# Kernel tuning notes

Hardware: AMD Instinct MI355X
Metric: run time of the kernel (lower is better)

The kernel has to match this reference:

```python
import jax, jax.numpy as jnp
import numpy as np

RADIUS = 5
KS = 2 * RADIUS - 1          # kernel_size = 9
PAD = KS // 2                # 4
CENTER = RADIUS - 1          # 4 (== PAD)
EPS = 1e-10


def _offsets_and_kernel():
    # Distance kernel exactly as torch.meshgrid(indexing='ij') in the module;
    # the center entry is skipped in the loop, so drop it here.
    yy, xx = np.meshgrid(np.arange(KS), np.arange(KS), indexing='ij')
    dist = np.sqrt((xx - CENTER) ** 2 + (yy - CENTER) ** 2).astype(np.float32)
    keep = ~((yy == CENTER) & (xx == CENTER))
    return (yy[keep].astype(np.int32), xx[keep].astype(np.int32), dist[keep])


def setup_inputs() -> dict:
    key = jax.random.key(0)
    target = (jax.random.uniform(key, (5, 2048, 2048)) < 0.15).astype(jnp.float32)
    return {"target": target}


def reference(target):
    # target: [5, H, W] binary float masks
    H, W = target.shape[1], target.shape[2]
    feature_weight = jnp.sum(target, axis=0)                      # [H, W]
    combined = (feature_weight > 0).astype(jnp.float32)           # [H, W]

    padded = jnp.pad(combined, PAD, mode='edge')                  # replicate pad
    oi, oj, kv = _offsets_and_kernel()
    offs = (jnp.asarray(oi), jnp.asarray(oj), jnp.asarray(kv))

    def body(min_d, off):
        i, j, k = off
        shifted = jax.lax.dynamic_slice(padded, (i, j), (H, W))
        diff = (shifted != combined).astype(jnp.float32)
        d = jnp.where(diff > 0, k / (diff + EPS), jnp.inf)
        return jnp.minimum(min_d, d), None

    min_d, _ = jax.lax.scan(body, jnp.full((H, W), jnp.inf, jnp.float32), offs)

    contour = jnp.where(jnp.isfinite(min_d), 1.0 / (min_d + EPS), 0.0)
    w = (feature_weight + contour) ** 2
    w = (w - w.min()) / (w.max() - w.min() + EPS)
    return w * combined
```

## Files before the change

### kernel.cpp

```cpp
#include <hip/hip_runtime.h>
#include <math.h>
#include <utility>

static constexpr int HH = 2048;
static constexpr int WW = 2048;
static constexpr int NPIX = HH * WW;
static constexpr int HPR = WW / 16;
static constexpr int TW = 256;
static constexpr int TH = 64;
static constexpr int GX = WW / TW;
static constexpr int GY = HH / TH;

template <typename F, int... Is>
__device__ __forceinline__ void sf_impl(F&& f, std::integer_sequence<int, Is...>) {
    (f(std::integral_constant<int, Is>{}), ...);
}
template <int N, typename F>
__device__ __forceinline__ void static_for(F&& f) {
    sf_impl(f, std::make_integer_sequence<int, N>{});
}

__host__ __device__ constexpr int rank_of(int d2) {
    switch (d2) {
        case 1:  return 1;  case 2:  return 2;  case 4:  return 3;
        case 5:  return 4;  case 8:  return 5;  case 9:  return 6;
        case 10: return 7;  case 13: return 8;  case 16: return 9;
        case 17: return 10; case 18: return 11; case 20: return 12;
        case 25: return 13; case 32: return 14;
    }
    return 0;
}

__device__ const int D2S[16] = {0, 1, 2, 4, 5, 8, 9, 10, 13, 16, 17, 18, 20, 25, 32, 0};

__device__ __forceinline__ unsigned long long spread8(unsigned int b) {
    unsigned long long t = (unsigned long long)b * 0x0101010101010101ull;
    t &= 0x8040201008040201ull;
    return ((t + 0x7f7f7f7f7f7f7f7full) >> 7) & 0x0101010101010101ull;
}

__global__ __launch_bounds__(512) void k_packdist(const float* __restrict__ t,
                                                  ulonglong2* __restrict__ code16,
                                                  unsigned long long* __restrict__ obs_blk) {
    __shared__ unsigned pkt[TH + 8][9];
    __shared__ unsigned char fwt[TH][TW];
    __shared__ unsigned long long swl[8], swh[8];

    const int bx = blockIdx.x & (GX - 1);
    const int by = blockIdx.x >> 3;
    const int tx0 = bx * TW, ty0 = by * TH;
    const int wid = threadIdx.x >> 6, lane = threadIdx.x & 63;

#pragma unroll 5
    for (int it = wid * 45; it < wid * 45 + 45; ++it) {
        const int r = it / 5;
        const int s = it - 5 * r;
        const bool active = (s < 4) | (lane < 8);
        const int c = (s < 4) ? (64 * s - 4 + lane) : (252 + lane);
        const int gy = min(max(ty0 + r - 4, 0), HH - 1);
        const int gx = min(max(tx0 + c, 0), WW - 1);
        float s5 = 0.f;
        if (active) {
            const int o = gy * WW + gx;
            s5 = t[o] + t[NPIX + o] + t[2 * NPIX + o] + t[3 * NPIX + o]
               + t[4 * NPIX + o];
        }
        const unsigned long long bal = __ballot(active && (s5 > 0.f));
        if (lane == 0) {
            if (s < 4) {
                pkt[r][2 * s]     = (unsigned)bal;
                pkt[r][2 * s + 1] = (unsigned)(bal >> 32);
            } else {
                pkt[r][8] = (unsigned)bal;
            }
        }
        const int rr = r - 4;
        if (active && rr >= 0 && rr < TH && c >= 0 && c < TW)
            fwt[rr][c] = (unsigned char)(int)s5;
    }
    __syncthreads();

    unsigned long long obl = 0, obh = 0;
#pragma unroll
    for (int k = 0; k < 2; ++k) {
        const int ch = threadIdx.x + k * 512;
        const int rr = ch >> 4;
        const int cx = ch & 15;
        const int x0 = cx * 16;
        const int w0 = x0 >> 5;
        const int sh = x0 & 31;

        unsigned acc[15];
        static_for<15>([&](auto I) { acc[I.value] = 0u; });

        const unsigned long long Wc =
            ((unsigned long long)pkt[rr + 4][w0]
           | ((unsigned long long)pkt[rr + 4][w0 + 1] << 32)) >> sh;
        const unsigned C = (unsigned)(Wc >> 4);

        static_for<9>([&](auto DY) {
            constexpr int dyi = DY.value;
            constexpr int dy = dyi - 4;
            const unsigned long long W = (dyi == 4) ? Wc :
                (((unsigned long long)pkt[rr + dyi][w0]
                | ((unsigned long long)pkt[rr + dyi][w0 + 1] << 32)) >> sh);
            static_for<9>([&](auto DX) {
                constexpr int dx = DX.value - 4;
                if constexpr (!(dx == 0 && dy == 0)) {
                    constexpr int rk = rank_of(dy * dy + dx * dx);
                    const unsigned S = (unsigned)(W >> (4 + dx));
                    acc[rk] |= S ^ C;
                }
            });
        });

        unsigned found = 0, p0 = 0, p1 = 0, p2 = 0, p3 = 0;
        static_for<14>([&](auto RI) {
            constexpr int r = RI.value + 1;
            const unsigned nw = acc[r] & ~found;
            found |= acc[r];
            if constexpr (r & 1) p0 |= nw;
            if constexpr (r & 2) p1 |= nw;
            if constexpr (r & 4) p2 |= nw;
            if constexpr (r & 8) p3 |= nw;
        });

        const uint4 fvw = *(const uint4*)&fwt[rr][x0];
        const unsigned long long fv0 =
            (unsigned long long)fvw.x | ((unsigned long long)fvw.y << 32);
        const unsigned long long fv1 =
            (unsigned long long)fvw.z | ((unsigned long long)fvw.w << 32);

        unsigned long long cq0 = 0, cq1 = 0;
        static_for<2>([&](auto J) {
            constexpr int j = J.value;
            const unsigned long long f = j ? fv1 : fv0;
            const unsigned c0 = (p0 >> (8 * j)) & 0xff;
            const unsigned c1 = (p1 >> (8 * j)) & 0xff;
            const unsigned c2 = (p2 >> (8 * j)) & 0xff;
            const unsigned c3 = (p3 >> (8 * j)) & 0xff;
            const unsigned long long cls = spread8(c0) | (spread8(c1) << 1)
                                         | (spread8(c2) << 2) | (spread8(c3) << 3);
            const unsigned long long cq = (f << 4) | cls;
            if constexpr (j == 0) cq0 = cq; else cq1 = cq;
            static_for<8>([&](auto B) {
                constexpr int b = B.value;
                const unsigned code = (unsigned)((cq >> (8 * b)) & 0xff);
                const unsigned long long bit = 1ull << (code & 63);
                const bool ishi = (code & 64) != 0;
                obl |= ishi ? 0ull : bit;
                obh |= ishi ? bit : 0ull;
            });
        });
        const int gchunk = (ty0 + rr) * HPR + bx * (TW / 16) + cx;
        code16[gchunk] = make_ulonglong2(cq0, cq1);
    }

#pragma unroll
    for (int s = 32; s > 0; s >>= 1) {
        obl |= __shfl_xor(obl, s);
        obh |= __shfl_xor(obh, s);
    }
    if (lane == 0) { swl[wid] = obl; swh[wid] = obh; }
    __syncthreads();
    if (threadIdx.x < 64) {
        unsigned long long l2 = (threadIdx.x < 8) ? swl[threadIdx.x] : 0ull;
        unsigned long long h2 = (threadIdx.x < 8) ? swh[threadIdx.x] : 0ull;
#pragma unroll
        for (int s = 4; s > 0; s >>= 1) {
            l2 |= __shfl_xor(l2, s);
            h2 |= __shfl_xor(h2, s);
        }
        if (threadIdx.x == 0) {
            obs_blk[blockIdx.x * 2]     = l2;
            obs_blk[blockIdx.x * 2 + 1] = h2;
        }
    }
}

__global__ __launch_bounds__(256) void k_out(const ulonglong2* __restrict__ code16,
                                             const unsigned long long* __restrict__ obs_blk,
                                             float* __restrict__ out) {
    __shared__ float tab[96];
    __shared__ float smn[4], smx[4];
    __shared__ unsigned long long slo[4], shi[4];

    const int tid = threadIdx.x;

    unsigned long long lo, hi;
    {
        const ulonglong2 s = ((const ulonglong2*)obs_blk)[tid];
        lo = s.x;
        hi = s.y;
#pragma unroll
        for (int s2 = 32; s2 > 0; s2 >>= 1) {
            lo |= __shfl_xor(lo, s2);
            hi |= __shfl_xor(hi, s2);
        }
        if ((tid & 63) == 0) { slo[tid >> 6] = lo; shi[tid >> 6] = hi; }
        __syncthreads();
        lo = slo[0] | slo[1] | slo[2] | slo[3];
        hi = shi[0] | shi[1] | shi[2] | shi[3];
    }

    float v = 0.f;
    bool present = false;
    if (tid < 96) {
        const int r = tid & 15;
        const float contour = (r >= 1 && r <= 14) ? 1.f / sqrtf((float)D2S[r]) : 0.f;
        const float t0 = (float)(tid >> 4) + contour;
        v = t0 * t0;
        present = (tid < 64) ? ((lo >> tid) & 1) : ((hi >> (tid - 64)) & 1);
    }
    float mnv = present ? v : INFINITY;
    float mxv = present ? v : -INFINITY;
#pragma unroll
    for (int s = 32; s > 0; s >>= 1) {
        mnv = fminf(mnv, __shfl_xor(mnv, s));
        mxv = fmaxf(mxv, __shfl_xor(mxv, s));
    }
    if ((tid & 63) == 0) { smn[tid >> 6] = mnv; smx[tid >> 6] = mxv; }
    __syncthreads();
    const float mn = fminf(fminf(smn[0], smn[1]), fminf(smn[2], smn[3]));
    const float mx = fmaxf(fmaxf(smx[0], smx[1]), fmaxf(smx[2], smx[3]));
    const float inv = 1.f / (mx - mn + 1e-10f);
    if (tid < 96) tab[tid] = (tid >= 16) ? (v - mn) * inv : 0.f;
    __syncthreads();

    const int t = blockIdx.x * 256 + tid;
    const ulonglong2 cq = code16[t];
    float4 v0, v1, v2, v3;
    v0.x = tab[(cq.x >> 0) & 0xff];  v0.y = tab[(cq.x >> 8) & 0xff];
    v0.z = tab[(cq.x >> 16) & 0xff]; v0.w = tab[(cq.x >> 24) & 0xff];
    v1.x = tab[(cq.x >> 32) & 0xff]; v1.y = tab[(cq.x >> 40) & 0xff];
    v1.z = tab[(cq.x >> 48) & 0xff]; v1.w = tab[(cq.x >> 56) & 0xff];
    v2.x = tab[(cq.y >> 0) & 0xff];  v2.y = tab[(cq.y >> 8) & 0xff];
    v2.z = tab[(cq.y >> 16) & 0xff]; v2.w = tab[(cq.y >> 24) & 0xff];
    v3.x = tab[(cq.y >> 32) & 0xff]; v3.y = tab[(cq.y >> 40) & 0xff];
    v3.z = tab[(cq.y >> 48) & 0xff]; v3.w = tab[(cq.y >> 56) & 0xff];
    const int ob = t * 16;
    *(float4*)(out + ob + 0)  = v0;
    *(float4*)(out + ob + 4)  = v1;
    *(float4*)(out + ob + 8)  = v2;
    *(float4*)(out + ob + 12) = v3;
}

extern "C" void kernel_launch(void* const* d_in, const int* in_sizes, int n_in,
                              void* d_out, int out_size, void* d_ws, size_t ws_size,
                              hipStream_t stream) {
    const float* target = (const float*)d_in[0];
    float* out = (float*)d_out;

    unsigned char* code = (unsigned char*)d_ws;
    unsigned long long* obs_blk = (unsigned long long*)(code + NPIX);

    k_packdist<<<GX * GY, 512, 0, stream>>>(
        target, (ulonglong2*)code, obs_blk);

    k_out<<<NPIX / 16 / 256, 256, 0, stream>>>(
        (const ulonglong2*)code, obs_blk, out);
}
```

Before: 45.25 us.

## Vectorize mask packing with float4 loads and 1024-thread blocks

The packing stage is rewritten so each thread loads 16 consecutive pixels from all five masks with float4 loads and builds a 16-bit row mask directly, replacing the per-lane scalar loads and wavefront ballots. The packed mask moves to 16-bit chunks, and the block grows to 1024 threads so each thread handles one 16-pixel output chunk instead of two. The goal is fewer memory instructions and better latency hiding on what is mainly a bandwidth-bound read of the five input masks. The trade-off is more registers per thread, which puts pressure on the requested occupancy, and a scalar fallback path for the chunks at the image edges.

```diff
diff --git a/kernel.cpp b/kernel.cpp
--- a/kernel.cpp
+++ b/kernel.cpp
@@ -10,6 +10,8 @@
 static constexpr int TH = 64;
 static constexpr int GX = WW / TW;
 static constexpr int GY = HH / TH;
+static constexpr int NCH = 18;
+static constexpr int NHR = TH + 8;
 
 template <typename F, int... Is>
 __device__ __forceinline__ void sf_impl(F&& f, std::integer_sequence<int, Is...>) {
@@ -39,135 +41,154 @@
     return ((t + 0x7f7f7f7f7f7f7f7full) >> 7) & 0x0101010101010101ull;
 }
 
-__global__ __launch_bounds__(512) void k_packdist(const float* __restrict__ t,
-                                                  ulonglong2* __restrict__ code16,
-                                                  unsigned long long* __restrict__ obs_blk) {
-    __shared__ unsigned pkt[TH + 8][9];
+__global__ __launch_bounds__(1024, 4) void k_packdist(
+        const float* __restrict__ t,
+        ulonglong2* __restrict__ code16,
+        unsigned long long* __restrict__ obs_blk) {
+    __shared__ unsigned short pk16[NHR][NCH];
     __shared__ unsigned char fwt[TH][TW];
-    __shared__ unsigned long long swl[8], swh[8];
+    __shared__ unsigned long long swl[16], swh[16];
 
     const int bx = blockIdx.x & (GX - 1);
     const int by = blockIdx.x >> 3;
     const int tx0 = bx * TW, ty0 = by * TH;
-    const int wid = threadIdx.x >> 6, lane = threadIdx.x & 63;
-
-#pragma unroll 5
-    for (int it = wid * 45; it < wid * 45 + 45; ++it) {
-        const int r = it / 5;
-        const int s = it - 5 * r;
-        const bool active = (s < 4) | (lane < 8);
-        const int c = (s < 4) ? (64 * s - 4 + lane) : (252 + lane);
+
+    for (int it = threadIdx.x; it < NHR * NCH; it += 1024) {
+        const int r = it / NCH;
+        const int cc = it - r * NCH;
         const int gy = min(max(ty0 + r - 4, 0), HH - 1);
-        const int gx = min(max(tx0 + c, 0), WW - 1);
-        float s5 = 0.f;
-        if (active) {
-            const int o = gy * WW + gx;
-            s5 = t[o] + t[NPIX + o] + t[2 * NPIX + o] + t[3 * NPIX + o]
-               + t[4 * NPIX + o];
-        }
-        const unsigned long long bal = __ballot(active && (s5 > 0.f));
-        if (lane == 0) {
-            if (s < 4) {
-                pkt[r][2 * s]     = (unsigned)bal;
-                pkt[r][2 * s + 1] = (unsigned)(bal >> 32);
-            } else {
-                pkt[r][8] = (unsigned)bal;
+        const int gxb = tx0 - 16 + cc * 16;
+        const float* __restrict__ p = t + (size_t)gy * WW + gxb;
+
+        unsigned bits = 0;
+        unsigned wq[4];
+        if (gxb >= 0 && gxb + 16 <= WW) {
+#pragma unroll
+            for (int i = 0; i < 4; ++i) {
+                const float4 a = *(const float4*)(p + 4 * i);
+                const float4 b = *(const float4*)(p + NPIX + 4 * i);
+                const float4 c = *(const float4*)(p + 2 * NPIX + 4 * i);
+                const float4 d = *(const float4*)(p + 3 * NPIX + 4 * i);
+                const float4 e = *(const float4*)(p + 4 * NPIX + 4 * i);
+                const float s0 = a.x + b.x + c.x + d.x + e.x;
+                const float s1 = a.y + b.y + c.y + d.y + e.y;
+                const float s2 = a.z + b.z + c.z + d.z + e.z;
+                const float s3 = a.w + b.w + c.w + d.w + e.w;
+                wq[i] = (unsigned)(int)s0 | ((unsigned)(int)s1 << 8)
+                      | ((unsigned)(int)s2 << 16) | ((unsigned)(int)s3 << 24);
+                bits |= ((s0 > 0.f) ? 1u : 0u) << (4 * i)
+                      | ((s1 > 0.f) ? 1u : 0u) << (4 * i + 1)
+                      | ((s2 > 0.f) ? 1u : 0u) << (4 * i + 2)
+                      | ((s3 > 0.f) ? 1u : 0u) << (4 * i + 3);
             }
-        }
+        } else {
+#pragma unroll
+            for (int i = 0; i < 4; ++i) {
+                unsigned w = 0;
+#pragma unroll
+                for (int j = 0; j < 4; ++j) {
+                    const int gx = min(max(gxb + 4 * i + j, 0), WW - 1);
+                    const size_t o = (size_t)gy * WW + gx;
+                    const float s = t[o] + t[NPIX + o] + t[2 * NPIX + o]
+                                  + t[3 * NPIX + o] + t[4 * NPIX + o];
+                    w |= ((unsigned)(int)s) << (8 * j);
+                    bits |= ((s > 0.f) ? 1u : 0u) << (4 * i + j);
+                }
+                wq[i] = w;
+            }
+        }
+        pk16[r][cc] = (unsigned short)bits;
         const int rr = r - 4;
-        if (active && rr >= 0 && rr < TH && c >= 0 && c < TW)
-            fwt[rr][c] = (unsigned char)(int)s5;
-    }
-    __syncthreads();
+        if (rr >= 0 && rr < TH && cc >= 1 && cc <= 16)
+            *(uint4*)&fwt[rr][(cc - 1) * 16] = make_uint4(wq[0], wq[1], wq[2], wq[3]);
+    }
+    __syncthreads();
+
+    const int rr = threadIdx.x >> 4;
+    const int cx = threadIdx.x & 15;
+    const int hc = cx + 1;
+
+    unsigned acc[15];
+    static_for<15>([&](auto I) { acc[I.value] = 0u; });
+
+    const unsigned long long Wc =
+        ((unsigned long long)pk16[rr + 4][hc - 1]
+       | ((unsigned long long)pk16[rr + 4][hc] << 16)
+       | ((unsigned long long)pk16[rr + 4][hc + 1] << 32)) >> 12;
+    const unsigned C = (unsigned)(Wc >> 4);
+
+    static_for<9>([&](auto DY) {
+        constexpr int dyi = DY.value;
+        constexpr int dy = dyi - 4;
+        const unsigned long long W = (dyi == 4) ? Wc :
+            (((unsigned long long)pk16[rr + dyi][hc - 1]
+            | ((unsigned long long)pk16[rr + dyi][hc] << 16)
+            | ((unsigned long long)pk16[rr + dyi][hc + 1] << 32)) >> 12);
+        static_for<9>([&](auto DX) {
+            constexpr int dx = DX.value - 4;
+            if constexpr (!(dx == 0 && dy == 0)) {
+                constexpr int rk = rank_of(dy * dy + dx * dx);
+                const unsigned S = (unsigned)(W >> (4 + dx));
+                acc[rk] |= S ^ C;
+            }
+        });
+    });
+
+    unsigned found = 0, p0 = 0, p1 = 0, p2 = 0, p3 = 0;
+    static_for<14>([&](auto RI) {
+        constexpr int r = RI.value + 1;
+        const unsigned nw = acc[r] & ~found;
+        found |= acc[r];
+        if constexpr (r & 1) p0 |= nw;
+        if constexpr (r & 2) p1 |= nw;
+        if constexpr (r & 4) p2 |= nw;
+        if constexpr (r & 8) p3 |= nw;
+    });
+
+    const uint4 fvw = *(const uint4*)&fwt[rr][cx * 16];
+    const unsigned long long fv0 =
+        (unsigned long long)fvw.x | ((unsigned long long)fvw.y << 32);
+    const unsigned long long fv1 =
+        (unsigned long long)fvw.z | ((unsigned long long)fvw.w << 32);
 
     unsigned long long obl = 0, obh = 0;
-#pragma unroll
-    for (int k = 0; k < 2; ++k) {
-        const int ch = threadIdx.x + k * 512;
-        const int rr = ch >> 4;
-        const int cx = ch & 15;
-        const int x0 = cx * 16;
-        const int w0 = x0 >> 5;
-        const int sh = x0 & 31;
-
-        unsigned acc[15];
-        static_for<15>([&](auto I) { acc[I.value] = 0u; });
-
-        const unsigned long long Wc =
-            ((unsigned long long)pkt[rr + 4][w0]
-           | ((unsigned long long)pkt[rr + 4][w0 + 1] << 32)) >> sh;
-        const unsigned C = (unsigned)(Wc >> 4);
-
-        static_for<9>([&](auto DY) {
-            constexpr int dyi = DY.value;
-            constexpr int dy = dyi - 4;
-            const unsigned long long W = (dyi == 4) ? Wc :
-                (((unsigned long long)pkt[rr + dyi][w0]
-                | ((unsigned long long)pkt[rr + dyi][w0 + 1] << 32)) >> sh);
-            static_for<9>([&](auto DX) {
-                constexpr int dx = DX.value - 4;
-                if constexpr (!(dx == 0 && dy == 0)) {
-                    constexpr int rk = rank_of(dy * dy + dx * dx);
-                    const unsigned S = (unsigned)(W >> (4 + dx));
-                    acc[rk] |= S ^ C;
-                }
-            });
+    unsigned long long cq0 = 0, cq1 = 0;
+    static_for<2>([&](auto J) {
+        constexpr int j = J.value;
+        const unsigned long long f = j ? fv1 : fv0;
+        const unsigned c0 = (p0 >> (8 * j)) & 0xff;
+        const unsigned c1 = (p1 >> (8 * j)) & 0xff;
+        const unsigned c2 = (p2 >> (8 * j)) & 0xff;
+        const unsigned c3 = (p3 >> (8 * j)) & 0xff;
+        const unsigned long long cls = spread8(c0) | (spread8(c1) << 1)
+                                     | (spread8(c2) << 2) | (spread8(c3) << 3);
+        const unsigned long long cq = (f << 4) | cls;
+        if constexpr (j == 0) cq0 = cq; else cq1 = cq;
+        static_for<8>([&](auto B) {
+            constexpr int b = B.value;
+            const unsigned code = (unsigned)((cq >> (8 * b)) & 0xff);
+            const unsigned long long bit = 1ull << (code & 63);
+            const bool ishi = (code & 64) != 0;
+            obl |= ishi ? 0ull : bit;
+            obh |= ishi ? bit : 0ull;
         });
-
-        unsigned found = 0, p0 = 0, p1 = 0, p2 = 0, p3 = 0;
-        static_for<14>([&](auto RI) {
-            constexpr int r = RI.value + 1;
-            const unsigned nw = acc[r] & ~found;
-            found |= acc[r];
-            if constexpr (r & 1) p0 |= nw;
-            if constexpr (r & 2) p1 |= nw;
-            if constexpr (r & 4) p2 |= nw;
-            if constexpr (r & 8) p3 |= nw;
-        });
-
-        const uint4 fvw = *(const uint4*)&fwt[rr][x0];
-        const unsigned long long fv0 =
-            (unsigned long long)fvw.x | ((unsigned long long)fvw.y << 32);
-        const unsigned long long fv1 =
-            (unsigned long long)fvw.z | ((unsigned long long)fvw.w << 32);
-
-        unsigned long long cq0 = 0, cq1 = 0;
-        static_for<2>([&](auto J) {
-            constexpr int j = J.value;
-            const unsigned long long f = j ? fv1 : fv0;
-            const unsigned c0 = (p0 >> (8 * j)) & 0xff;
-            const unsigned c1 = (p1 >> (8 * j)) & 0xff;
-            const unsigned c2 = (p2 >> (8 * j)) & 0xff;
-            const unsigned c3 = (p3 >> (8 * j)) & 0xff;
-            const unsigned long long cls = spread8(c0) | (spread8(c1) << 1)
-                                         | (spread8(c2) << 2) | (spread8(c3) << 3);
-            const unsigned long long cq = (f << 4) | cls;
-            if constexpr (j == 0) cq0 = cq; else cq1 = cq;
-            static_for<8>([&](auto B) {
-                constexpr int b = B.value;
-                const unsigned code = (unsigned)((cq >> (8 * b)) & 0xff);
-                const unsigned long long bit = 1ull << (code & 63);
-                const bool ishi = (code & 64) != 0;
-                obl |= ishi ? 0ull : bit;
-                obh |= ishi ? bit : 0ull;
-            });
-        });
-        const int gchunk = (ty0 + rr) * HPR + bx * (TW / 16) + cx;
-        code16[gchunk] = make_ulonglong2(cq0, cq1);
-    }
+    });
+    const int gchunk = (ty0 + rr) * HPR + bx * (TW / 16) + cx;
+    code16[gchunk] = make_ulonglong2(cq0, cq1);
 
 #pragma unroll
     for (int s = 32; s > 0; s >>= 1) {
         obl |= __shfl_xor(obl, s);
         obh |= __shfl_xor(obh, s);
     }
+    const int wid = threadIdx.x >> 6, lane = threadIdx.x & 63;
     if (lane == 0) { swl[wid] = obl; swh[wid] = obh; }
     __syncthreads();
     if (threadIdx.x < 64) {
-        unsigned long long l2 = (threadIdx.x < 8) ? swl[threadIdx.x] : 0ull;
-        unsigned long long h2 = (threadIdx.x < 8) ? swh[threadIdx.x] : 0ull;
-#pragma unroll
-        for (int s = 4; s > 0; s >>= 1) {
+        unsigned long long l2 = (threadIdx.x < 16) ? swl[threadIdx.x] : 0ull;
+        unsigned long long h2 = (threadIdx.x < 16) ? swh[threadIdx.x] : 0ull;
+#pragma unroll
+        for (int s = 8; s > 0; s >>= 1) {
             l2 |= __shfl_xor(l2, s);
             h2 |= __shfl_xor(h2, s);
         }
@@ -254,7 +275,7 @@
     unsigned char* code = (unsigned char*)d_ws;
     unsigned long long* obs_blk = (unsigned long long*)(code + NPIX);
 
-    k_packdist<<<GX * GY, 512, 0, stream>>>(
+    k_packdist<<<GX * GY, 1024, 0, stream>>>(
         target, (ulonglong2*)code, obs_blk);
 
     k_out<<<NPIX / 16 / 256, 256, 0, stream>>>(
```

Result: faster. 43.40 us (-4.1%).
